# Optimization experiments

Measured on AMD Instinct MI355X. Metric: run time of the kernel, lower is better.

Reference implementation:

```python
import jax, jax.numpy as jnp
import numpy as np
from jax import lax

D_MODEL = 2048
D_STATE = 16
D_CONV = 4
B_SZ = 2
T_LEN = 2048


def setup_inputs() -> dict:
    key = jax.random.key(0)
    ks = jax.random.split(key, 8)
    x = jax.random.normal(ks[0], (B_SZ, T_LEN, D_MODEL), dtype=jnp.float32)
    h = jnp.zeros((B_SZ, D_MODEL, D_STATE), dtype=jnp.float32)
    norm_w = jnp.ones((D_MODEL,), dtype=jnp.float32)
    in_proj_w = jax.random.normal(ks[1], (2 * D_MODEL, D_MODEL), dtype=jnp.float32) * (D_MODEL ** -0.5)
    conv_w = jax.random.normal(ks[2], (D_MODEL, 1, D_CONV), dtype=jnp.float32) * 0.5
    conv_b = jnp.zeros((D_MODEL,), dtype=jnp.float32)
    x_proj_w = jax.random.normal(ks[3], (D_MODEL + 2 * D_STATE, D_MODEL), dtype=jnp.float32) * (D_MODEL ** -0.5)
    A_log = jnp.broadcast_to(jnp.log(jnp.arange(1, D_STATE + 1, dtype=jnp.float32))[None, :], (D_MODEL, D_STATE)).copy()
    D = jnp.ones((D_MODEL,), dtype=jnp.float32)
    out_proj_w = jax.random.normal(ks[4], (D_MODEL, D_MODEL), dtype=jnp.float32) * (D_MODEL ** -0.5)
    return {"x": x, "h": h, "norm_w": norm_w, "in_proj_w": in_proj_w,
            "conv_w": conv_w, "conv_b": conv_b, "x_proj_w": x_proj_w,
            "A_log": A_log, "D": D, "out_proj_w": out_proj_w}


def _rmsnorm(x, w, eps=1e-6):
    ms = jnp.mean(jnp.square(x.astype(jnp.float32)), axis=-1, keepdims=True)
    return (x * lax.rsqrt(ms + eps).astype(x.dtype)) * w.astype(x.dtype)


def reference(x, h, norm_w, in_proj_w, conv_w, conv_b, x_proj_w, A_log, D, out_proj_w):
    B, T, d_model = x.shape
    d_state = A_log.shape[1]
    residual = x
    x_normed = _rmsnorm(x, norm_w)
    xz = x_normed @ in_proj_w.T                      # (B, T, 2*d_model)
    x_branch, z = jnp.split(xz, 2, axis=-1)
    # depthwise causal conv1d: torch pads both sides by d_conv-1 then slices [:T],
    # equivalent to left-pad-only causal conv.
    xc = x_branch.transpose(0, 2, 1)                 # (B, d_model, T)
    xc = lax.conv_general_dilated(
        xc, conv_w, window_strides=(1,), padding=[(D_CONV - 1, 0)],
        dimension_numbers=("NCH", "OIH", "NCH"), feature_group_count=d_model)
    xc = xc + conv_b[None, :, None]
    x_ssm = jax.nn.silu(xc.transpose(0, 2, 1))       # (B, T, d_model)

    # SSM core
    proj = x_ssm @ x_proj_w.T                        # (B, T, d_model + 2*d_state)
    delta_raw = proj[..., :d_model]
    B_in = proj[..., d_model:d_model + d_state]
    C_in = proj[..., d_model + d_state:]
    delta = jax.nn.softplus(delta_raw)               # (B, T, d_model)
    A = -jnp.exp(A_log.astype(jnp.float32))          # (d_model, d_state)

    def step(h_c, inp):
        d_t, b_t, c_t, x_t = inp                     # (B,dm) (B,ds) (B,ds) (B,dm)
        A_bar = jnp.exp(d_t[:, :, None] * A[None])   # (B, dm, ds)
        h_c = A_bar * h_c + (d_t * x_t)[:, :, None] * b_t[:, None, :]
        y_t = jnp.einsum("bdn,bn->bd", h_c, c_t) + D * x_t
        return h_c, y_t

    xs = (delta.transpose(1, 0, 2), B_in.transpose(1, 0, 2),
          C_in.transpose(1, 0, 2), x_ssm.transpose(1, 0, 2))
    h_new, ys = lax.scan(step, h.astype(x.dtype), xs)
    y = ys.transpose(1, 0, 2)                        # (B, T, d_model)

    y = y * jax.nn.silu(z)
    out = residual + y @ out_proj_w.T
    return out, lax.stop_gradient(h_new)
```

## Files before the change

### kernel.cpp

```cpp
#include <hip/hip_runtime.h>
#include <cstdint>
#include <cstddef>


typedef __bf16 bf16_t;
typedef __attribute__((ext_vector_type(8))) __bf16 bf16x8;
typedef __attribute__((ext_vector_type(4))) __bf16 bf16x4;
typedef __attribute__((ext_vector_type(4))) float f32x4;

#define D_MODEL 2048
#define D_STATE 16
#define B_SZ 2
#define T_LEN 2048
#define N_ROWS (B_SZ * T_LEN)
#define N_PAD  2304
#define N_CHUNK 32
#define L_CHUNK (T_LEN / N_CHUNK)
#define LOG2E 1.4426950408889634f

__device__ __forceinline__ void load_lds16(const void* g, void* l) {
    __builtin_amdgcn_global_load_lds(
        (const __attribute__((address_space(1))) void*)(uintptr_t)g,
        (__attribute__((address_space(3))) void*)(uintptr_t)l,
        16, 0, 0);
}

#define VMW(n) asm volatile("s_waitcnt vmcnt(" #n ")" ::: "memory")
#define BAR()  do { __builtin_amdgcn_s_barrier(); __builtin_amdgcn_sched_barrier(0); } while (0)

__global__ __launch_bounds__(256) void cast_w13(
    const float* __restrict__ w1, const float* __restrict__ w3,
    bf16_t* __restrict__ d1, bf16_t* __restrict__ d3)
{
    int i = blockIdx.x * 256 + threadIdx.x;
    const int n1 = 4096 * 2048 / 4;
    if (i < n1) {
        f32x4 v = ((const f32x4*)w1)[i];
        ((bf16x4*)d1)[i] = __builtin_convertvector(v, bf16x4);
    } else {
        int j = i - n1;
        f32x4 v = ((const f32x4*)w3)[j];
        ((bf16x4*)d3)[j] = __builtin_convertvector(v, bf16x4);
    }
}

__global__ __launch_bounds__(256) void cast_pad_w2(
    const float* __restrict__ s, bf16_t* __restrict__ d)
{
    int i = blockIdx.x * 256 + threadIdx.x;
    int row = i >> 11;
    int col = i & 2047;
    float v = (row < 2080) ? s[(size_t)row * 2048 + col] : 0.f;
    d[i] = (bf16_t)v;
}

__global__ __launch_bounds__(256) void rmsnorm_kernel(
    const float* __restrict__ x, const float* __restrict__ w,
    bf16_t* __restrict__ xn)
{
    int row = blockIdx.x;
    int tid = threadIdx.x;
    const f32x4* xr = (const f32x4*)(x + (size_t)row * D_MODEL);
    f32x4 v0 = xr[tid];
    f32x4 v1 = xr[tid + 256];
    float ss = 0.f;
    #pragma unroll
    for (int e = 0; e < 4; ++e) { ss = fmaf(v0[e], v0[e], ss); ss = fmaf(v1[e], v1[e], ss); }
    #pragma unroll
    for (int o = 32; o > 0; o >>= 1) ss += __shfl_down(ss, o, 64);
    __shared__ float red[4];
    if ((tid & 63) == 0) red[tid >> 6] = ss;
    __syncthreads();
    float tot = red[0] + red[1] + red[2] + red[3];
    float scale = rsqrtf(tot * (1.f / D_MODEL) + 1e-6f);
    const f32x4* w4 = (const f32x4*)w;
    f32x4 m0 = v0 * w4[tid] * scale;
    f32x4 m1 = v1 * w4[tid + 256] * scale;
    bf16x4* xo = (bf16x4*)(xn + (size_t)row * D_MODEL);
    xo[tid]       = __builtin_convertvector(m0, bf16x4);
    xo[tid + 256] = __builtin_convertvector(m1, bf16x4);
}

template<int MODE>
__global__ __launch_bounds__(512, 2) void gemm_bt(
    const bf16_t* __restrict__ A, const bf16_t* __restrict__ Bw, int K,
    float* __restrict__ out0, bf16_t* __restrict__ out1,
    const float* __restrict__ add)
{
    __shared__ __align__(16) char smem[131072];
    char* const ldsA = smem;
    char* const ldsB = smem + 65536;

    const int tid  = threadIdx.x;
    const int nwg = gridDim.x * gridDim.y;
    const int lin = blockIdx.x + gridDim.x * blockIdx.y;
    const int wg  = (lin & 7) * (nwg >> 3) + (lin >> 3);
    const int bm  = wg & 15;
    const int bn  = wg >> 4;

    const int lane = tid & 63;
    const int wave = tid >> 6;
    const int wm   = wave >> 2;
    const int wn   = wave & 3;
    const int fr   = lane & 15;
    const int quad = lane >> 4;

    const int rS   = tid >> 2;
    const int cS   = tid & 3;
    const int gcol = ((cS - ((rS >> 1) & 3)) & 3) * 8;
    const bf16_t* sA0 = A  + (size_t)(bm * 256 + rS) * K + gcol;
    const bf16_t* sA1 = sA0 + (size_t)128 * K;
    const bf16_t* sB0 = Bw + (size_t)(bn * 256 + rS) * K + gcol;
    const bf16_t* sB1 = sB0 + (size_t)128 * K;

    const int swz  = ((quad + ((fr >> 1) & 3)) & 3) * 8;
    const int aOff = (wm * 128 + fr) * 32 + swz;
    const int bOff = (wn * 64  + fr) * 32 + swz;

    f32x4 acc[8][4];
    #pragma unroll
    for (int i = 0; i < 8; ++i)
        #pragma unroll
        for (int j = 0; j < 4; ++j) acc[i][j] = {0.f, 0.f, 0.f, 0.f};

#define SL0(b) load_lds16(sA0, ldsA + (b) * 16384 + tid * 16)
#define SL1(b) load_lds16(sA1, ldsA + (b) * 16384 + tid * 16 + 8192)
#define SL2(b) load_lds16(sB0, ldsB + (b) * 16384 + tid * 16)
#define SL3(b) load_lds16(sB1, ldsB + (b) * 16384 + tid * 16 + 8192)
#define ADV()  do { sA0 += 32; sA1 += 32; sB0 += 32; sB1 += 32; } while (0)

#define PHASE(cb, p, SLX)                                                     \
    {                                                                         \
        const bf16_t* pA = (const bf16_t*)(ldsA + (cb) * 16384);              \
        bf16x8 aLo = *(const bf16x8*)(pA + aOff + (2 * (p)) * 512);           \
        bf16x8 aHi = *(const bf16x8*)(pA + aOff + (2 * (p) + 1) * 512);       \
        SLX;                                                                  \
        BAR();                                                                \
        __builtin_amdgcn_s_setprio(1);                                        \
        _Pragma("unroll")                                                     \
        for (int j = 0; j < 4; ++j)                                           \
            acc[2 * (p)][j] = __builtin_amdgcn_mfma_f32_16x16x32_bf16(        \
                aLo, bfr[j], acc[2 * (p)][j], 0, 0, 0);                       \
        _Pragma("unroll")                                                     \
        for (int j = 0; j < 4; ++j)                                           \
            acc[2 * (p) + 1][j] = __builtin_amdgcn_mfma_f32_16x16x32_bf16(    \
                aHi, bfr[j], acc[2 * (p) + 1][j], 0, 0, 0);                   \
        __builtin_amdgcn_s_setprio(0);                                        \
    }

#define TILE(cb, nb, ST)                                                      \
    {                                                                         \
        const bf16_t* pB = (const bf16_t*)(ldsB + (cb) * 16384);              \
        bf16x8 bfr[4];                                                        \
        _Pragma("unroll")                                                     \
        for (int j = 0; j < 4; ++j)                                           \
            bfr[j] = *(const bf16x8*)(pB + bOff + j * 512);                   \
        PHASE(cb, 0, if (ST) SL0(nb))                                         \
        PHASE(cb, 1, if (ST) SL1(nb))                                         \
        PHASE(cb, 2, if (ST) SL2(nb))                                         \
        PHASE(cb, 3, if (ST) { SL3(nb); ADV(); })                             \
    }

    const int nt = K >> 5;
    SL0(0); SL1(0); SL2(0); SL3(0); ADV();
    SL0(1); SL1(1); SL2(1); SL3(1); ADV();
    SL0(2); SL1(2); SL2(2); SL3(2); ADV();
    for (int t = 0; t < nt - 3; ++t) {
        VMW(8); BAR();
        TILE(t & 3, (t + 3) & 3, true)
    }
    VMW(8); BAR(); TILE((nt - 3) & 3, 0, false)
    VMW(4); BAR(); TILE((nt - 2) & 3, 0, false)
    VMW(0); BAR(); TILE((nt - 1) & 3, 0, false)
#undef SL0
#undef SL1
#undef SL2
#undef SL3
#undef ADV
#undef PHASE
#undef TILE

    float* const cs = (float*)smem;
    __syncthreads();
    for (int s = 0; s < 4; ++s) {
        if (wm == (s >> 1)) {
            const int i0 = (s & 1) * 4;
            #pragma unroll
            for (int ii = 0; ii < 4; ++ii)
                #pragma unroll
                for (int j = 0; j < 4; ++j)
                    #pragma unroll
                    for (int rr = 0; rr < 4; ++rr)
                        cs[(ii * 16 + quad * 4 + rr) * 268 + wn * 64 + j * 16 + fr]
                            = acc[i0 + ii][j][rr];
        }
        __syncthreads();
        #pragma unroll
        for (int k = 0; k < 8; ++k) {
            const int idx = tid + k * 512;
            const int row = idx >> 6;
            const int c4  = (idx & 63) << 2;
            f32x4 v = *(const f32x4*)(cs + row * 268 + c4);
            const int gr = bm * 256 + s * 64 + row;
            const int gc = bn * 256 + c4;
            if (MODE == 0) {
                if (bn < 8) {
                    *(f32x4*)&out0[(size_t)gr * 2048 + gc] = v;
                } else {
                    bf16x4 o;
                    #pragma unroll
                    for (int e = 0; e < 4; ++e) {
                        float sv = v[e];
                        o[e] = (bf16_t)(sv / (1.f + __expf(-sv)));
                    }
                    *(bf16x4*)&out1[(size_t)gr * 2048 + (gc - 2048)] = o;
                }
            } else if (MODE == 1) {
                if (bn < 8) {
                    #pragma unroll
                    for (int e = 0; e < 4; ++e) {
                        float sv = v[e];
                        v[e] = fmaxf(sv, 0.f) + __logf(1.f + __expf(-fabsf(sv)));
                    }
                }
                *(f32x4*)&out0[(size_t)gr * N_PAD + gc] = v;
            } else {
                f32x4 a4 = *(const f32x4*)&add[(size_t)gr * 2048 + gc];
                *(f32x4*)&out0[(size_t)gr * 2048 + gc] = v + a4;
            }
        }
        __syncthreads();
    }
}

__global__ __launch_bounds__(256) void conv_silu_kernel(
    const float* __restrict__ xb, const float* __restrict__ cw,
    const float* __restrict__ cb, bf16_t* __restrict__ xs_b)
{
    int id = blockIdx.x * 256 + threadIdx.x;
    int d  = id & 2047;
    int tb = (id >> 11) & 255;
    int b  = id >> 19;
    float w0 = cw[d * 4 + 0], w1 = cw[d * 4 + 1], w2 = cw[d * 4 + 2], w3 = cw[d * 4 + 3];
    float bias = cb[d];
    int t0 = tb * 8;
    size_t base = (size_t)b * T_LEN;
    float v[11];
    #pragma unroll
    for (int i = 0; i < 11; ++i) {
        int t = t0 - 3 + i;
        v[i] = (t >= 0) ? xb[(base + t) * 2048 + d] : 0.f;
    }
    #pragma unroll
    for (int j = 0; j < 8; ++j) {
        float s = bias + w0 * v[j] + w1 * v[j + 1] + w2 * v[j + 2] + w3 * v[j + 3];
        float sl = s / (1.f + __expf(-s));
        xs_b[(base + t0 + j) * D_MODEL + d] = (bf16_t)sl;
    }
}

#define PF 4

__global__ __launch_bounds__(256) void scan_phase1(
    const float* __restrict__ proj, const bf16_t* __restrict__ xs,
    const float* __restrict__ A_log,
    float* __restrict__ Aprod, float* __restrict__ hfin)
{
    int wi   = blockIdx.x * 4 + (threadIdx.x >> 6);
    int lane = threadIdx.x & 63;
    int nq   = lane & 3;
    int dsub = lane >> 2;
    int c  = wi & 31;
    int dg = (wi >> 5) & 127;
    int b  = wi >> 12;
    int dd = dg * 16 + dsub;

    float A2[4], h[4], Ap[4];
    #pragma unroll
    for (int j = 0; j < 4; ++j) {
        A2[j] = -__expf(A_log[dd * D_STATE + nq * 4 + j]) * LOG2E;
        h[j] = 0.f; Ap[j] = 1.f;
    }
    const int t0 = c * L_CHUNK;
    const int tmax = t0 + L_CHUNK - 1;

    float p_da[PF], p_xv[PF];
    f32x4 p_B[PF];
    #pragma unroll
    for (int u = 0; u < PF; ++u) {
        size_t row = (size_t)b * T_LEN + t0 + u;
        const float* pr = proj + row * N_PAD;
        p_da[u] = pr[dd];
        p_xv[u] = (float)xs[row * D_MODEL + dd];
        p_B[u]  = *(const f32x4*)(pr + D_MODEL + nq * 4);
    }

    for (int it = 0; it < L_CHUNK; it += PF) {
        #pragma unroll
        for (int u = 0; u < PF; ++u) {
            int t = t0 + it + u;
            float da = p_da[u], xv = p_xv[u];
            f32x4 Bv = p_B[u];
            int tn = t + PF; tn = (tn > tmax) ? tmax : tn;
            {
                size_t row = (size_t)b * T_LEN + tn;
                const float* pr = proj + row * N_PAD;
                p_da[u] = pr[dd];
                p_xv[u] = (float)xs[row * D_MODEL + dd];
                p_B[u]  = *(const f32x4*)(pr + D_MODEL + nq * 4);
            }
            float dx = da * xv;
            #pragma unroll
            for (int j = 0; j < 4; ++j) {
                float a = exp2f(da * A2[j]);
                Ap[j] *= a;
                h[j] = fmaf(a, h[j], dx * Bv[j]);
            }
        }
    }
    size_t o = ((size_t)c * 4096 + b * 2048 + dd) * D_STATE + nq * 4;
    *(f32x4*)(Aprod + o) = f32x4{Ap[0], Ap[1], Ap[2], Ap[3]};
    *(f32x4*)(hfin  + o) = f32x4{h[0], h[1], h[2], h[3]};
}

__global__ __launch_bounds__(256) void scan_phase2(
    const float* __restrict__ h_in, const float* __restrict__ Aprod,
    float* __restrict__ hfin, float* __restrict__ h_out)
{
    int g = blockIdx.x * 256 + threadIdx.x;
    float h = h_in[g];
    for (int c = 0; c < N_CHUNK; ++c) {
        size_t o = (size_t)c * 65536 + g;
        float a   = Aprod[o];
        float loc = hfin[o];
        hfin[o] = h;
        h = fmaf(a, h, loc);
    }
    h_out[g] = h;
}

__global__ __launch_bounds__(256) void scan_phase3(
    const float* __restrict__ proj, const bf16_t* __restrict__ xs,
    const bf16_t* __restrict__ zg, const float* __restrict__ A_log,
    const float* __restrict__ Dv, const float* __restrict__ hinit,
    bf16_t* __restrict__ yg)
{
    int wi   = blockIdx.x * 4 + (threadIdx.x >> 6);
    int lane = threadIdx.x & 63;
    int nq   = lane & 3;
    int dsub = lane >> 2;
    int c  = wi & 31;
    int dg = (wi >> 5) & 127;
    int b  = wi >> 12;
    int dd = dg * 16 + dsub;

    float A2[4], h[4];
    size_t o = ((size_t)c * 4096 + b * 2048 + dd) * D_STATE + nq * 4;
    #pragma unroll
    for (int j = 0; j < 4; ++j) {
        A2[j] = -__expf(A_log[dd * D_STATE + nq * 4 + j]) * LOG2E;
        h[j]  = hinit[o + j];
    }
    float Dd = Dv[dd];
    const int t0 = c * L_CHUNK;
    const int tmax = t0 + L_CHUNK - 1;

    float p_da[PF], p_xv[PF], p_sz[PF];
    f32x4 p_B[PF], p_C[PF];
    #pragma unroll
    for (int u = 0; u < PF; ++u) {
        size_t row = (size_t)b * T_LEN + t0 + u;
        const float* pr = proj + row * N_PAD;
        p_da[u] = pr[dd];
        p_xv[u] = (float)xs[row * D_MODEL + dd];
        p_sz[u] = (float)zg[row * 2048 + dd];
        p_B[u]  = *(const f32x4*)(pr + D_MODEL + nq * 4);
        p_C[u]  = *(const f32x4*)(pr + D_MODEL + D_STATE + nq * 4);
    }

    for (int it = 0; it < L_CHUNK; it += PF) {
        #pragma unroll
        for (int u = 0; u < PF; ++u) {
            int t = t0 + it + u;
            float da = p_da[u], xv = p_xv[u], sz = p_sz[u];
            f32x4 Bv = p_B[u], Cv = p_C[u];
            int tn = t + PF; tn = (tn > tmax) ? tmax : tn;
            {
                size_t row = (size_t)b * T_LEN + tn;
                const float* pr = proj + row * N_PAD;
                p_da[u] = pr[dd];
                p_xv[u] = (float)xs[row * D_MODEL + dd];
                p_sz[u] = (float)zg[row * 2048 + dd];
                p_B[u]  = *(const f32x4*)(pr + D_MODEL + nq * 4);
                p_C[u]  = *(const f32x4*)(pr + D_MODEL + D_STATE + nq * 4);
            }
            float dx = da * xv;
            float yp = 0.f;
            #pragma unroll
            for (int j = 0; j < 4; ++j) {
                float a = exp2f(da * A2[j]);
                h[j] = fmaf(a, h[j], dx * Bv[j]);
                yp = fmaf(h[j], Cv[j], yp);
            }
            yp += __shfl_xor(yp, 1, 64);
            yp += __shfl_xor(yp, 2, 64);
            if (nq == 0) {
                float y = fmaf(Dd, xv, yp);
                yg[((size_t)b * T_LEN + t) * D_MODEL + dd] = (bf16_t)(y * sz);
            }
        }
    }
}

extern "C" void kernel_launch(void* const* d_in, const int* in_sizes, int n_in,
                              void* d_out, int out_size, void* d_ws, size_t ws_size,
                              hipStream_t stream)
{
    const float* x    = (const float*)d_in[0];
    const float* h0   = (const float*)d_in[1];
    const float* nw   = (const float*)d_in[2];
    const float* w_in = (const float*)d_in[3];
    const float* cw   = (const float*)d_in[4];
    const float* cb   = (const float*)d_in[5];
    const float* w_x  = (const float*)d_in[6];
    const float* alog = (const float*)d_in[7];
    const float* dv   = (const float*)d_in[8];
    const float* w_out= (const float*)d_in[9];
    float* out  = (float*)d_out;
    float* hout = out + (size_t)N_ROWS * D_MODEL;

    char* ws = (char*)d_ws;
    size_t off = 0;
    auto alloc = [&](size_t bytes) -> void* {
        void* p = ws + off;
        off += (bytes + 255) & ~(size_t)255;
        return p;
    };
    bf16_t* W1  = (bf16_t*)alloc((size_t)4096 * 2048 * 2);
    bf16_t* W2  = (bf16_t*)alloc((size_t)N_PAD * 2048 * 2);
    bf16_t* W3  = (bf16_t*)alloc((size_t)2048 * 2048 * 2);
    bf16_t* XN  = (bf16_t*)alloc((size_t)N_ROWS * 2048 * 2);
    float*  XB  = (float*) alloc((size_t)N_ROWS * 2048 * 4);
    bf16_t* ZG  = (bf16_t*)alloc((size_t)N_ROWS * 2048 * 2);
    float*  PROJ= (float*) alloc((size_t)N_ROWS * N_PAD * 4);
    float* APROD= (float*) alloc((size_t)N_CHUNK * 4096 * D_STATE * 4);
    float* HFIN = (float*) alloc((size_t)N_CHUNK * 4096 * D_STATE * 4);
    bf16_t* XSb = W1;
    bf16_t* YG  = XN;

    cast_w13<<<(4096 * 2048 / 4 + 2048 * 2048 / 4) / 256, 256, 0, stream>>>(w_in, w_out, W1, W3);
    cast_pad_w2<<<(N_PAD * 2048) / 256, 256, 0, stream>>>(w_x, W2);

    rmsnorm_kernel<<<N_ROWS, 256, 0, stream>>>(x, nw, XN);
    gemm_bt<0><<<dim3(16, 16), 512, 0, stream>>>(XN, W1, 2048, XB, ZG, nullptr);
    conv_silu_kernel<<<(B_SZ * (T_LEN / 8) * D_MODEL) / 256, 256, 0, stream>>>(XB, cw, cb, XSb);
    gemm_bt<1><<<dim3(16, N_PAD / 256), 512, 0, stream>>>(XSb, W2, 2048, PROJ, nullptr, nullptr);
    scan_phase1<<<2048, 256, 0, stream>>>(PROJ, XSb, alog, APROD, HFIN);
    scan_phase2<<<256, 256, 0, stream>>>(h0, APROD, HFIN, hout);
    scan_phase3<<<2048, 256, 0, stream>>>(PROJ, XSb, ZG, alog, dv, HFIN, YG);
    gemm_bt<2><<<dim3(16, 8), 512, 0, stream>>>(YG, W3, 2048, out, nullptr, x);

    (void)in_sizes; (void)n_in; (void)out_size; (void)ws_size;
}
```

Before: 536.5 us.

## Restructure GEMM main loop into double-buffered 64-wide K tiles with 8-phase schedule

Replaces the 4-deep ring of 32-wide K tiles with two 64 KB buffers, each holding two 32-wide K sub-slices of A and B. The loop runs 8 phases per 128-K iteration, each doing 16 MFMAs while issuing one global-to-LDS stage, with vmcnt waits and two barriers per phase. The aim is to overlap loads with compute more evenly and cut per-tile barrier overhead. In exchange it adds more barriers per phase and shallower prefetch depth, and the tail handling and wait counts must line up exactly.

New measurement: 470.0 us. -12.4%, faster.

```diff
diff --git a/kernel.cpp b/kernel.cpp
--- a/kernel.cpp
+++ b/kernel.cpp
@@ -88,8 +88,8 @@
     const float* __restrict__ add)
 {
     __shared__ __align__(16) char smem[131072];
-    char* const ldsA = smem;
-    char* const ldsB = smem + 65536;
+    char* const ldsAp = smem;
+    char* const ldsBp = smem + 32768;
 
     const int tid  = threadIdx.x;
     const int nwg = gridDim.x * gridDim.y;
@@ -108,10 +108,8 @@
     const int rS   = tid >> 2;
     const int cS   = tid & 3;
     const int gcol = ((cS - ((rS >> 1) & 3)) & 3) * 8;
-    const bf16_t* sA0 = A  + (size_t)(bm * 256 + rS) * K + gcol;
-    const bf16_t* sA1 = sA0 + (size_t)128 * K;
-    const bf16_t* sB0 = Bw + (size_t)(bn * 256 + rS) * K + gcol;
-    const bf16_t* sB1 = sB0 + (size_t)128 * K;
+    const bf16_t* pAg = A  + (size_t)(bm * 256 + rS) * K + gcol;
+    const bf16_t* pBg = Bw + (size_t)(bn * 256 + rS) * K + gcol;
 
     const int swz  = ((quad + ((fr >> 1) & 3)) & 3) * 8;
     const int aOff = (wm * 128 + fr) * 32 + swz;
@@ -123,68 +121,88 @@
         #pragma unroll
         for (int j = 0; j < 4; ++j) acc[i][j] = {0.f, 0.f, 0.f, 0.f};
 
-#define SL0(b) load_lds16(sA0, ldsA + (b) * 16384 + tid * 16)
-#define SL1(b) load_lds16(sA1, ldsA + (b) * 16384 + tid * 16 + 8192)
-#define SL2(b) load_lds16(sB0, ldsB + (b) * 16384 + tid * 16)
-#define SL3(b) load_lds16(sB1, ldsB + (b) * 16384 + tid * 16 + 8192)
-#define ADV()  do { sA0 += 32; sA1 += 32; sB0 += 32; sB1 += 32; } while (0)
-
-#define PHASE(cb, p, SLX)                                                     \
+    bf16x8 bfr[4];
+
+#define STG_A(b, t, s) do { \
+        const bf16_t* g_ = pAg + (t) * 64 + (s) * 32; \
+        char* l_ = ldsAp + (b) * 65536 + (s) * 16384 + tid * 16; \
+        load_lds16(g_, l_); load_lds16(g_ + (size_t)128 * K, l_ + 8192); } while (0)
+#define STG_B(b, t, s) do { \
+        const bf16_t* g_ = pBg + (t) * 64 + (s) * 32; \
+        char* l_ = ldsBp + (b) * 65536 + (s) * 16384 + tid * 16; \
+        load_lds16(g_, l_); load_lds16(g_ + (size_t)128 * K, l_ + 8192); } while (0)
+
+#define PHASE(BUF, S, IH, STAGE_STMT, TAIL_STMT)                              \
     {                                                                         \
-        const bf16_t* pA = (const bf16_t*)(ldsA + (cb) * 16384);              \
-        bf16x8 aLo = *(const bf16x8*)(pA + aOff + (2 * (p)) * 512);           \
-        bf16x8 aHi = *(const bf16x8*)(pA + aOff + (2 * (p) + 1) * 512);       \
-        SLX;                                                                  \
+        const bf16_t* pA_ = (const bf16_t*)(ldsAp + (BUF)*65536 + (S)*16384); \
+        if ((IH) == 0) {                                                      \
+            const bf16_t* pB_ =                                               \
+                (const bf16_t*)(ldsBp + (BUF)*65536 + (S)*16384);             \
+            _Pragma("unroll")                                                 \
+            for (int j = 0; j < 4; ++j)                                       \
+                bfr[j] = *(const bf16x8*)(pB_ + bOff + j * 512);              \
+        }                                                                     \
+        bf16x8 af0 = *(const bf16x8*)(pA_ + aOff + ((IH)*4 + 0) * 512);       \
+        bf16x8 af1 = *(const bf16x8*)(pA_ + aOff + ((IH)*4 + 1) * 512);       \
+        bf16x8 af2 = *(const bf16x8*)(pA_ + aOff + ((IH)*4 + 2) * 512);       \
+        bf16x8 af3 = *(const bf16x8*)(pA_ + aOff + ((IH)*4 + 3) * 512);       \
+        STAGE_STMT;                                                           \
         BAR();                                                                \
         __builtin_amdgcn_s_setprio(1);                                        \
         _Pragma("unroll")                                                     \
         for (int j = 0; j < 4; ++j)                                           \
-            acc[2 * (p)][j] = __builtin_amdgcn_mfma_f32_16x16x32_bf16(        \
-                aLo, bfr[j], acc[2 * (p)][j], 0, 0, 0);                       \
+            acc[(IH)*4+0][j] = __builtin_amdgcn_mfma_f32_16x16x32_bf16(       \
+                af0, bfr[j], acc[(IH)*4+0][j], 0, 0, 0);                      \
         _Pragma("unroll")                                                     \
         for (int j = 0; j < 4; ++j)                                           \
-            acc[2 * (p) + 1][j] = __builtin_amdgcn_mfma_f32_16x16x32_bf16(    \
-                aHi, bfr[j], acc[2 * (p) + 1][j], 0, 0, 0);                   \
-        __builtin_amdgcn_s_setprio(0);                                        \
-    }
-
-#define TILE(cb, nb, ST)                                                      \
-    {                                                                         \
-        const bf16_t* pB = (const bf16_t*)(ldsB + (cb) * 16384);              \
-        bf16x8 bfr[4];                                                        \
+            acc[(IH)*4+1][j] = __builtin_amdgcn_mfma_f32_16x16x32_bf16(       \
+                af1, bfr[j], acc[(IH)*4+1][j], 0, 0, 0);                      \
         _Pragma("unroll")                                                     \
         for (int j = 0; j < 4; ++j)                                           \
-            bfr[j] = *(const bf16x8*)(pB + bOff + j * 512);                   \
-        PHASE(cb, 0, if (ST) SL0(nb))                                         \
-        PHASE(cb, 1, if (ST) SL1(nb))                                         \
-        PHASE(cb, 2, if (ST) SL2(nb))                                         \
-        PHASE(cb, 3, if (ST) { SL3(nb); ADV(); })                             \
-    }
-
-    const int nt = K >> 5;
-    SL0(0); SL1(0); SL2(0); SL3(0); ADV();
-    SL0(1); SL1(1); SL2(1); SL3(1); ADV();
-    SL0(2); SL1(2); SL2(2); SL3(2); ADV();
-    for (int t = 0; t < nt - 3; ++t) {
-        VMW(8); BAR();
-        TILE(t & 3, (t + 3) & 3, true)
-    }
-    VMW(8); BAR(); TILE((nt - 3) & 3, 0, false)
-    VMW(4); BAR(); TILE((nt - 2) & 3, 0, false)
-    VMW(0); BAR(); TILE((nt - 1) & 3, 0, false)
-#undef SL0
-#undef SL1
-#undef SL2
-#undef SL3
-#undef ADV
+            acc[(IH)*4+2][j] = __builtin_amdgcn_mfma_f32_16x16x32_bf16(       \
+                af2, bfr[j], acc[(IH)*4+2][j], 0, 0, 0);                      \
+        _Pragma("unroll")                                                     \
+        for (int j = 0; j < 4; ++j)                                           \
+            acc[(IH)*4+3][j] = __builtin_amdgcn_mfma_f32_16x16x32_bf16(       \
+                af3, bfr[j], acc[(IH)*4+3][j], 0, 0, 0);                      \
+        __builtin_amdgcn_s_setprio(0);                                        \
+        TAIL_STMT;                                                            \
+        BAR();                                                                \
+    }
+
+    STG_B(0, 0, 0); STG_A(0, 0, 0); STG_B(0, 0, 1); STG_A(0, 0, 1);
+    STG_B(1, 1, 0); STG_A(1, 1, 0); STG_B(1, 1, 1);
+    VMW(10); BAR();
+
+    const int NI = K >> 7;
+    for (int I = 0; I < NI - 1; ++I) {
+        const int t2 = 2 * I + 2, t3 = 2 * I + 3;
+        PHASE(0, 0, 0, STG_A(1, t2 - 1, 1), (void)0)
+        PHASE(0, 0, 1, STG_B(0, t2, 0),     VMW(10))
+        PHASE(0, 1, 0, STG_A(0, t2, 0),     (void)0)
+        PHASE(0, 1, 1, STG_B(0, t2, 1),     VMW(10))
+        PHASE(1, 0, 0, STG_A(0, t2, 1),     (void)0)
+        PHASE(1, 0, 1, STG_B(1, t3, 0),     VMW(10))
+        PHASE(1, 1, 0, STG_A(1, t3, 0),     (void)0)
+        PHASE(1, 1, 1, STG_B(1, t3, 1),     VMW(10))
+    }
+    PHASE(0, 0, 0, STG_A(1, 2 * NI - 1, 1), (void)0)
+    PHASE(0, 0, 1, (void)0, VMW(8))
+    PHASE(0, 1, 0, (void)0, (void)0)
+    PHASE(0, 1, 1, (void)0, VMW(4))
+    PHASE(1, 0, 0, (void)0, (void)0)
+    PHASE(1, 0, 1, (void)0, VMW(0))
+    PHASE(1, 1, 0, (void)0, (void)0)
+    PHASE(1, 1, 1, (void)0, (void)0)
+#undef STG_A
+#undef STG_B
 #undef PHASE
-#undef TILE
 
     float* const cs = (float*)smem;
     __syncthreads();
+    #pragma unroll
     for (int s = 0; s < 4; ++s) {
         if (wm == (s >> 1)) {
-            const int i0 = (s & 1) * 4;
             #pragma unroll
             for (int ii = 0; ii < 4; ++ii)
                 #pragma unroll
@@ -192,7 +210,7 @@
                     #pragma unroll
                     for (int rr = 0; rr < 4; ++rr)
                         cs[(ii * 16 + quad * 4 + rr) * 268 + wn * 64 + j * 16 + fr]
-                            = acc[i0 + ii][j][rr];
+                            = acc[(s & 1) * 4 + ii][j][rr];
         }
         __syncthreads();
         #pragma unroll
```
